# Kernel tuning notes

Measured on AMD Instinct MI355X. Metric: run time of the kernel, lower is better.

## Reference

```python
import jax, jax.numpy as jnp
import numpy as np

# ---- constants mirroring the torch module ----
LOSS_ALPHA = 1.0      # args.loss_weight_alpha (intra-class weight)
LOSS_BETA = 1.0       # args.loss_weight_beta (focal weight)
FOCAL_GAMMA = 2.0
FOCAL_ALPHA = 0.85
EPS = 1e-09
LDAM_S = 30.0
CLS_NUM = np.array([85.0, 900.0])
LDAM_MAX_M = 0.5
LDAM_W = np.array([0.15, 0.85], dtype=np.float32)
B = 16777216


def setup_inputs() -> dict:
    key = jax.random.key(0)
    k1, k2 = jax.random.split(key)
    x = jax.random.uniform(k1, (B, 2), dtype=jnp.float32)  # [B, 2] probabilities-like logits
    target = jax.random.randint(k2, (B,), 0, 2)            # binary labels
    return {"x": x, "target": target}


def _intraclass_p(centered, std, target, cls):
    # correlation between consecutive same-class rows (sorted-index order),
    # vectorized: class-c indices first via stable argsort, mask invalid pairs.
    n_rows = centered.shape[0]
    mask = target == cls
    n = jnp.sum(mask)
    order = jnp.argsort(jnp.where(mask, jnp.arange(n_rows), n_rows))
    a, b = order[:-1], order[1:]
    corr = jnp.sum(centered[a] * centered[b], axis=1) / (std[a] * std[b])
    valid = jnp.arange(n_rows - 1) < (n - 1)
    s = jnp.sum(jnp.where(valid, corr, 0.0))
    return jnp.where(n > 0, s / jnp.maximum(n, 1).astype(s.dtype), 0.0)


def reference(x, target):
    num_cls = x.shape[1]
    # ---- LDAM loss ----
    m = 1.0 / np.sqrt(np.sqrt(CLS_NUM))
    m = m * (LDAM_MAX_M / np.max(m))
    m_list = jnp.asarray(m, jnp.float32)
    w = jnp.asarray(LDAM_W)
    batch_m = m_list[target]                                      # [B]
    onehot = jax.nn.one_hot(target, num_cls, dtype=bool)          # [B, C]
    out = jnp.where(onehot, x - batch_m[:, None], x)              # margin on target logit only
    logsm = jax.nn.log_softmax(LDAM_S * out, axis=-1)
    nll = -jnp.take_along_axis(logsm, target[:, None], axis=1)[:, 0]
    wi = w[target]
    ldam = jnp.sum(wi * nll) / jnp.sum(wi)                        # weighted-mean cross entropy
    # ---- binary focal loss (treats x[:,1] as probability) ----
    p = x[:, 1]
    t = target.astype(x.dtype)
    fl = (-FOCAL_ALPHA * t * (1.0 - p) ** FOCAL_GAMMA * jnp.log(p + EPS)
          - (1.0 - FOCAL_ALPHA) * (1.0 - t) * p ** FOCAL_GAMMA * jnp.log(1.0 - p + EPS))
    focal = jnp.mean(fl)
    # ---- intra-class correlation loss ----
    centered = x - jnp.mean(x, axis=1, keepdims=True)
    std = jnp.std(x, axis=1, ddof=1)                               # torch.std default: unbiased
    p0 = _intraclass_p(centered, std, target, 0)
    p1 = _intraclass_p(centered, std, target, 1)
    intra = (p0 - p1) ** 2
    return ldam + LOSS_BETA * focal + LOSS_ALPHA * intra
```

## Files before the change

### kernel.cpp

```cpp
#include <hip/hip_runtime.h>

#define E_BLOCK 8192
#define E_WAVE  2048
#define ITERS   16

#define M1      0.2771814156f
#define LDAM_S  30.0f

struct BlockRec {
  int s0, p0, s1, p1;
  float wnll, fl;
  int cnt1, pad;
};

__device__ __forceinline__ void comb(int &sa, int &pa, int sb, int pb) {
  if (pa == 0) { sa = sb; pa = pb; }
  else if (pb != 0) {
    int la = ((pa >> 1) & 1) * 2 - 1;
    int fb = (pb & 1) * 2 - 1;
    sa += sb + la * fb;
    pa = 4 | (pa & 1) | (pb & 2);
  }
}

__global__ __launch_bounds__(256) void loss_pass1(
    const float* __restrict__ x, const int* __restrict__ tgt,
    BlockRec* __restrict__ recs, int B) {
  const int w    = threadIdx.x >> 6;
  const int lane = threadIdx.x & 63;
  const int waveBase = blockIdx.x * E_BLOCK + w * E_WAVE;

  float wnll = 0.f, fls = 0.f;
  int cnt1 = 0;
  int rs0 = 0, rp0 = 0, rs1 = 0, rp1 = 0;

  for (int j = 0; j < ITERS; ++j) {
    const int e = waveBase + ((j << 6) + lane) * 2;
    int ps0 = 0, pp0 = 0, ps1 = 0, pp1 = 0;
    if (e < B) {
      const float4 xv = *reinterpret_cast<const float4*>(x + 2 * e);
      const int2  tv = *reinterpret_cast<const int2*>(tgt + e);
      int sA, sB;
      {
        const float x0 = xv.x, x1 = xv.y; const int t = tv.x;
        const float d  = t ? LDAM_S * (x0 - x1 + M1) : LDAM_S * (x1 - x0 + 0.5f);
        const float sp = fmaxf(d, 0.f) + __logf(1.f + __expf(-fabsf(d)));
        wnll += (t ? 0.85f : 0.15f) * sp;
        fls  += t ? (-0.85f * (1.f - x1) * (1.f - x1) * __logf(x1 + 1e-9f))
                  : (-0.15f * x1 * x1 * __logf(1.f - x1 + 1e-9f));
        cnt1 += t;
        sA = (x0 > x1) ? 1 : -1;
      }
      {
        const float x0 = xv.z, x1 = xv.w; const int t = tv.y;
        const float d  = t ? LDAM_S * (x0 - x1 + M1) : LDAM_S * (x1 - x0 + 0.5f);
        const float sp = fmaxf(d, 0.f) + __logf(1.f + __expf(-fabsf(d)));
        wnll += (t ? 0.85f : 0.15f) * sp;
        fls  += t ? (-0.85f * (1.f - x1) * (1.f - x1) * __logf(x1 + 1e-9f))
                  : (-0.15f * x1 * x1 * __logf(1.f - x1 + 1e-9f));
        cnt1 += t;
        sB = (x0 > x1) ? 1 : -1;
      }
      const int bA = (sA > 0), bB = (sB > 0);
      const bool a0 = (tv.x == 0), b0 = (tv.y == 0);
      if (a0 && b0)      { ps0 = sA * sB; pp0 = 4 | bA | (bB << 1); }
      else if (a0)       { pp0 = 4 | bA | (bA << 1); }
      else if (b0)       { pp0 = 4 | bB | (bB << 1); }
      if (!a0 && !b0)    { ps1 = sA * sB; pp1 = 4 | bA | (bB << 1); }
      else if (!a0)      { pp1 = 4 | bA | (bA << 1); }
      else if (!b0)      { pp1 = 4 | bB | (bB << 1); }
    }
    #pragma unroll
    for (int k = 0; k < 6; ++k) {
      const int m = 1 << k;
      const int os0 = __shfl_xor(ps0, m), op0 = __shfl_xor(pp0, m);
      const int os1 = __shfl_xor(ps1, m), op1 = __shfl_xor(pp1, m);
      const bool up = (lane & m) != 0;
      int fs = up ? os0 : ps0, fp = up ? op0 : pp0;
      int gs = up ? ps0 : os0, gp = up ? pp0 : op0;
      comb(fs, fp, gs, gp); ps0 = fs; pp0 = fp;
      fs = up ? os1 : ps1; fp = up ? op1 : pp1;
      gs = up ? ps1 : os1; gp = up ? pp1 : op1;
      comb(fs, fp, gs, gp); ps1 = fs; pp1 = fp;
    }
    comb(rs0, rp0, ps0, pp0);
    comb(rs1, rp1, ps1, pp1);
  }

  #pragma unroll
  for (int k = 1; k < 64; k <<= 1) {
    wnll += __shfl_xor(wnll, k);
    fls  += __shfl_xor(fls, k);
    cnt1 += __shfl_xor(cnt1, k);
  }

  __shared__ int   shi[4][5];
  __shared__ float shf[4][2];
  if (lane == 0) {
    shi[w][0] = rs0; shi[w][1] = rp0; shi[w][2] = rs1; shi[w][3] = rp1; shi[w][4] = cnt1;
    shf[w][0] = wnll; shf[w][1] = fls;
  }
  __syncthreads();
  if (threadIdx.x == 0) {
    int S0 = 0, P0 = 0, S1 = 0, P1 = 0, C = 0; float W = 0.f, F = 0.f;
    #pragma unroll
    for (int q = 0; q < 4; ++q) {
      comb(S0, P0, shi[q][0], shi[q][1]);
      comb(S1, P1, shi[q][2], shi[q][3]);
      C += shi[q][4]; W += shf[q][0]; F += shf[q][1];
    }
    BlockRec r; r.s0 = S0; r.p0 = P0; r.s1 = S1; r.p1 = P1;
    r.wnll = W; r.fl = F; r.cnt1 = C; r.pad = 0;
    recs[blockIdx.x] = r;
  }
}

__global__ __launch_bounds__(64) void loss_pass2(
    const BlockRec* __restrict__ recs, int NB, int B, float* __restrict__ out) {
  const int lane = threadIdx.x;
  const int G = (NB + 63) >> 6;
  int s0 = 0, p0 = 0, s1 = 0, p1 = 0;
  double W = 0.0, F = 0.0;
  long long C = 0;
  for (int g = 0; g < G; ++g) {
    const int b = lane * G + g;
    if (b < NB) {
      const BlockRec r = recs[b];
      comb(s0, p0, r.s0, r.p0);
      comb(s1, p1, r.s1, r.p1);
      W += (double)r.wnll; F += (double)r.fl; C += r.cnt1;
    }
  }
  #pragma unroll
  for (int k = 0; k < 6; ++k) {
    const int m = 1 << k;
    const int os0 = __shfl_xor(s0, m), op0 = __shfl_xor(p0, m);
    const int os1 = __shfl_xor(s1, m), op1 = __shfl_xor(p1, m);
    const double oW = __shfl_xor(W, m), oF = __shfl_xor(F, m);
    const long long oC = __shfl_xor(C, m);
    const bool up = (lane & m) != 0;
    int fs = up ? os0 : s0, fp = up ? op0 : p0;
    int gs = up ? s0 : os0, gp = up ? p0 : op0;
    comb(fs, fp, gs, gp); s0 = fs; p0 = fp;
    fs = up ? os1 : s1; fp = up ? op1 : p1;
    gs = up ? s1 : os1; gp = up ? p1 : op1;
    comb(fs, fp, gs, gp); s1 = fs; p1 = fp;
    W += oW; F += oF; C += oC;
  }
  if (lane == 0) {
    const double n1 = (double)C, n0 = (double)B - n1;
    const double sw = 0.15 * n0 + 0.85 * n1;
    const double ldam  = W / sw;
    const double focal = F / (double)B;
    const double q0 = (n0 > 0.0) ? (double)s0 / n0 : 0.0;
    const double q1 = (n1 > 0.0) ? (double)s1 / n1 : 0.0;
    const double dq = q0 - q1;
    out[0] = (float)(ldam + focal + dq * dq);
  }
}

extern "C" void kernel_launch(void* const* d_in, const int* in_sizes, int n_in,
                              void* d_out, int out_size, void* d_ws, size_t ws_size,
                              hipStream_t stream) {
  const float* x  = (const float*)d_in[0];
  const int* tgt  = (const int*)d_in[1];
  float* out      = (float*)d_out;
  const int B  = in_sizes[1];
  const int NB = (B + E_BLOCK - 1) / E_BLOCK;
  BlockRec* recs = (BlockRec*)d_ws;
  loss_pass1<<<NB, 256, 0, stream>>>(x, tgt, recs, B);
  loss_pass2<<<1, 64, 0, stream>>>(recs, NB, B, out);
}
```

Measured before the change: 254.2 us.

## Replace per-iteration wave scans with LDS-staged sequential per-thread chain reduction

Each element's sign and class are now packed into a byte and staged in shared memory. Each thread then walks a contiguous chunk of 32 elements sequentially to build per-class (sum, first, last) chain summaries. This replaces the six-step shuffle butterfly that previously ran every iteration. The second pass widens to 256 threads with a shared-memory stage and a simpler first/last combine. The aim is to cut shuffle and branch cost in the hot loop, at the price of LDS traffic and extra barriers.

```diff
diff --git a/kernel.cpp b/kernel.cpp
--- a/kernel.cpp
+++ b/kernel.cpp
@@ -13,149 +13,178 @@
   int cnt1, pad;
 };
 
-__device__ __forceinline__ void comb(int &sa, int &pa, int sb, int pb) {
-  if (pa == 0) { sa = sb; pa = pb; }
-  else if (pb != 0) {
-    int la = ((pa >> 1) & 1) * 2 - 1;
-    int fb = (pb & 1) * 2 - 1;
-    sa += sb + la * fb;
-    pa = 4 | (pa & 1) | (pb & 2);
-  }
+__device__ __forceinline__ void comb0(int &s, int &f, int &l, int sb, int fb, int lb) {
+  s += sb + l * fb;
+  f = f ? f : fb;
+  l = fb ? lb : l;
+}
+
+__device__ __forceinline__ void bfly_step(int m, int lane, int &s, int &f, int &l) {
+  const int os = __shfl_xor(s, m), of = __shfl_xor(f, m), ol = __shfl_xor(l, m);
+  const bool up = (lane & m) != 0;
+  int as = up ? os : s, af = up ? of : f, al = up ? ol : l;
+  const int bs = up ? s : os, bf = up ? f : of, bl = up ? l : ol;
+  comb0(as, af, al, bs, bf, bl);
+  s = as; f = af; l = al;
 }
 
 __global__ __launch_bounds__(256) void loss_pass1(
     const float* __restrict__ x, const int* __restrict__ tgt,
     BlockRec* __restrict__ recs, int B) {
-  const int w    = threadIdx.x >> 6;
-  const int lane = threadIdx.x & 63;
+  __shared__ unsigned int lds[3328];
+  unsigned int* chunkw = lds;
+  unsigned int* stw = lds + 2304;
+  float* wnw = (float*)(lds + 2560);
+  float* flw = (float*)(lds + 2816);
+  int*   cnw = (int*)(lds + 3072);
+  unsigned short* cs = (unsigned short*)lds;
+
+  const int tid = threadIdx.x;
+  const int w = tid >> 6, lane = tid & 63;
   const int waveBase = blockIdx.x * E_BLOCK + w * E_WAVE;
 
-  float wnll = 0.f, fls = 0.f;
-  int cnt1 = 0;
-  int rs0 = 0, rp0 = 0, rs1 = 0, rp1 = 0;
+  float wnll = 0.f, fls = 0.f; int cnt1 = 0;
 
   for (int j = 0; j < ITERS; ++j) {
     const int e = waveBase + ((j << 6) + lane) * 2;
-    int ps0 = 0, pp0 = 0, ps1 = 0, pp1 = 0;
+    unsigned int pk = 0;
     if (e < B) {
       const float4 xv = *reinterpret_cast<const float4*>(x + 2 * e);
       const int2  tv = *reinterpret_cast<const int2*>(tgt + e);
-      int sA, sB;
+      unsigned int c[2];
+      const float x0a = xv.x, x1a = xv.y; const float x0b = xv.z, x1b = xv.w;
+      const int ta = tv.x, tb = tv.y;
       {
-        const float x0 = xv.x, x1 = xv.y; const int t = tv.x;
-        const float d  = t ? LDAM_S * (x0 - x1 + M1) : LDAM_S * (x1 - x0 + 0.5f);
-        const float sp = fmaxf(d, 0.f) + __logf(1.f + __expf(-fabsf(d)));
-        wnll += (t ? 0.85f : 0.15f) * sp;
-        fls  += t ? (-0.85f * (1.f - x1) * (1.f - x1) * __logf(x1 + 1e-9f))
-                  : (-0.15f * x1 * x1 * __logf(1.f - x1 + 1e-9f));
-        cnt1 += t;
-        sA = (x0 > x1) ? 1 : -1;
+        const float d  = x0a - x1a;
+        const float z  = LDAM_S * (ta ? (d + M1) : (0.5f - d));
+        const float sp = fmaxf(z, 0.f) + __logf(1.f + __expf(-fabsf(z)));
+        wnll += (ta ? 0.85f : 0.15f) * sp;
+        const float p  = x1a;
+        const float lg = __logf((ta ? p : (1.f - p)) + 1e-9f);
+        const float cf = ta ? (-0.85f * (1.f - p) * (1.f - p)) : (-0.15f * p * p);
+        fls += cf * lg;
+        cnt1 += ta;
+        c[0] = 4u | (unsigned)(x0a > x1a) | ((unsigned)ta << 1);
       }
       {
-        const float x0 = xv.z, x1 = xv.w; const int t = tv.y;
-        const float d  = t ? LDAM_S * (x0 - x1 + M1) : LDAM_S * (x1 - x0 + 0.5f);
-        const float sp = fmaxf(d, 0.f) + __logf(1.f + __expf(-fabsf(d)));
-        wnll += (t ? 0.85f : 0.15f) * sp;
-        fls  += t ? (-0.85f * (1.f - x1) * (1.f - x1) * __logf(x1 + 1e-9f))
-                  : (-0.15f * x1 * x1 * __logf(1.f - x1 + 1e-9f));
-        cnt1 += t;
-        sB = (x0 > x1) ? 1 : -1;
+        const float d  = x0b - x1b;
+        const float z  = LDAM_S * (tb ? (d + M1) : (0.5f - d));
+        const float sp = fmaxf(z, 0.f) + __logf(1.f + __expf(-fabsf(z)));
+        wnll += (tb ? 0.85f : 0.15f) * sp;
+        const float p  = x1b;
+        const float lg = __logf((tb ? p : (1.f - p)) + 1e-9f);
+        const float cf = tb ? (-0.85f * (1.f - p) * (1.f - p)) : (-0.15f * p * p);
+        fls += cf * lg;
+        cnt1 += tb;
+        c[1] = 4u | (unsigned)(x0b > x1b) | ((unsigned)tb << 1);
       }
-      const int bA = (sA > 0), bB = (sB > 0);
-      const bool a0 = (tv.x == 0), b0 = (tv.y == 0);
-      if (a0 && b0)      { ps0 = sA * sB; pp0 = 4 | bA | (bB << 1); }
-      else if (a0)       { pp0 = 4 | bA | (bA << 1); }
-      else if (b0)       { pp0 = 4 | bB | (bB << 1); }
-      if (!a0 && !b0)    { ps1 = sA * sB; pp1 = 4 | bA | (bB << 1); }
-      else if (!a0)      { pp1 = 4 | bA | (bA << 1); }
-      else if (!b0)      { pp1 = 4 | bB | (bB << 1); }
+      pk = c[0] | (c[1] << 8);
+    }
+    const int li2 = w * 1024 + (j << 6) + lane;
+    cs[(li2 >> 4) * 18 + (li2 & 15)] = (unsigned short)pk;
+  }
+  __syncthreads();
+
+  int s0 = 0, f0 = 0, l0 = 0, s1 = 0, f1 = 0, l1 = 0;
+  #pragma unroll
+  for (int r = 0; r < 8; ++r) {
+    const unsigned int wv = chunkw[tid * 9 + r];
+    #pragma unroll
+    for (int k = 0; k < 4; ++k) {
+      const unsigned int b = (wv >> (8 * k)) & 7u;
+      if (b & 4u) {
+        const int sv = (int)((b & 1u) << 1) - 1;
+        const int t  = (int)((b >> 1) & 1u);
+        const int lv = t ? l1 : l0;
+        const int add = lv * sv;
+        if (t) { s1 += add; l1 = sv; f1 = f1 ? f1 : sv; }
+        else   { s0 += add; l0 = sv; f0 = f0 ? f0 : sv; }
+      }
+    }
+  }
+  stw[tid] = (unsigned)(s0 + 128) | ((unsigned)(f0 + 1) << 8) | ((unsigned)(l0 + 1) << 10)
+           | ((unsigned)(s1 + 128) << 16) | ((unsigned)(f1 + 1) << 24) | ((unsigned)(l1 + 1) << 26);
+  wnw[tid] = wnll; flw[tid] = fls; cnw[tid] = cnt1;
+  __syncthreads();
+
+  if (w == 0) {
+    int S0 = 0, F0 = 0, L0 = 0, S1 = 0, F1 = 0, L1 = 0;
+    float W = 0.f, F = 0.f; int C = 0;
+    #pragma unroll
+    for (int q = 0; q < 4; ++q) {
+      const int i = lane * 4 + q;
+      const unsigned int pk = stw[i];
+      comb0(S0, F0, L0, (int)(pk & 255u) - 128, (int)((pk >> 8) & 3u) - 1, (int)((pk >> 10) & 3u) - 1);
+      comb0(S1, F1, L1, (int)((pk >> 16) & 255u) - 128, (int)((pk >> 24) & 3u) - 1, (int)((pk >> 26) & 3u) - 1);
+      W += wnw[i]; F += flw[i]; C += cnw[i];
     }
     #pragma unroll
     for (int k = 0; k < 6; ++k) {
       const int m = 1 << k;
-      const int os0 = __shfl_xor(ps0, m), op0 = __shfl_xor(pp0, m);
-      const int os1 = __shfl_xor(ps1, m), op1 = __shfl_xor(pp1, m);
-      const bool up = (lane & m) != 0;
-      int fs = up ? os0 : ps0, fp = up ? op0 : pp0;
-      int gs = up ? ps0 : os0, gp = up ? pp0 : op0;
-      comb(fs, fp, gs, gp); ps0 = fs; pp0 = fp;
-      fs = up ? os1 : ps1; fp = up ? op1 : pp1;
-      gs = up ? ps1 : os1; gp = up ? pp1 : op1;
-      comb(fs, fp, gs, gp); ps1 = fs; pp1 = fp;
-    }
-    comb(rs0, rp0, ps0, pp0);
-    comb(rs1, rp1, ps1, pp1);
-  }
-
-  #pragma unroll
-  for (int k = 1; k < 64; k <<= 1) {
-    wnll += __shfl_xor(wnll, k);
-    fls  += __shfl_xor(fls, k);
-    cnt1 += __shfl_xor(cnt1, k);
-  }
-
-  __shared__ int   shi[4][5];
-  __shared__ float shf[4][2];
-  if (lane == 0) {
-    shi[w][0] = rs0; shi[w][1] = rp0; shi[w][2] = rs1; shi[w][3] = rp1; shi[w][4] = cnt1;
-    shf[w][0] = wnll; shf[w][1] = fls;
-  }
+      bfly_step(m, lane, S0, F0, L0);
+      bfly_step(m, lane, S1, F1, L1);
+      W += __shfl_xor(W, m); F += __shfl_xor(F, m); C += __shfl_xor(C, m);
+    }
+    if (lane == 0) {
+      BlockRec r;
+      r.s0 = S0; r.p0 = (F0 + 1) | ((L0 + 1) << 4);
+      r.s1 = S1; r.p1 = (F1 + 1) | ((L1 + 1) << 4);
+      r.wnll = W; r.fl = F; r.cnt1 = C; r.pad = 0;
+      recs[blockIdx.x] = r;
+    }
+  }
+}
+
+__global__ __launch_bounds__(256) void loss_pass2(
+    const BlockRec* __restrict__ recs, int NB, int B, float* __restrict__ out) {
+  __shared__ int sS0[256], sF0[256], sL0[256], sS1[256], sF1[256], sL1[256], sC[256];
+  __shared__ double sW[256], sFl[256];
+  const int tid = threadIdx.x, w = tid >> 6, lane = tid & 63;
+  const int R = (NB + 255) >> 8;
+
+  int s0 = 0, f0 = 0, l0 = 0, s1 = 0, f1 = 0, l1 = 0;
+  double W = 0.0, Fd = 0.0; int C = 0;
+  for (int r = 0; r < R; ++r) {
+    const int b = tid * R + r;
+    if (b < NB) {
+      const BlockRec rec = recs[b];
+      comb0(s0, f0, l0, rec.s0, (rec.p0 & 3) - 1, ((rec.p0 >> 4) & 3) - 1);
+      comb0(s1, f1, l1, rec.s1, (rec.p1 & 3) - 1, ((rec.p1 >> 4) & 3) - 1);
+      W += (double)rec.wnll; Fd += (double)rec.fl; C += rec.cnt1;
+    }
+  }
+  sS0[tid] = s0; sF0[tid] = f0; sL0[tid] = l0;
+  sS1[tid] = s1; sF1[tid] = f1; sL1[tid] = l1;
+  sC[tid] = C; sW[tid] = W; sFl[tid] = Fd;
   __syncthreads();
-  if (threadIdx.x == 0) {
-    int S0 = 0, P0 = 0, S1 = 0, P1 = 0, C = 0; float W = 0.f, F = 0.f;
+
+  if (w == 0) {
+    int S0 = 0, F0 = 0, L0 = 0, S1 = 0, F1 = 0, L1 = 0; int Ct = 0;
+    double Wt = 0.0, Ft = 0.0;
     #pragma unroll
     for (int q = 0; q < 4; ++q) {
-      comb(S0, P0, shi[q][0], shi[q][1]);
-      comb(S1, P1, shi[q][2], shi[q][3]);
-      C += shi[q][4]; W += shf[q][0]; F += shf[q][1];
-    }
-    BlockRec r; r.s0 = S0; r.p0 = P0; r.s1 = S1; r.p1 = P1;
-    r.wnll = W; r.fl = F; r.cnt1 = C; r.pad = 0;
-    recs[blockIdx.x] = r;
-  }
-}
-
-__global__ __launch_bounds__(64) void loss_pass2(
-    const BlockRec* __restrict__ recs, int NB, int B, float* __restrict__ out) {
-  const int lane = threadIdx.x;
-  const int G = (NB + 63) >> 6;
-  int s0 = 0, p0 = 0, s1 = 0, p1 = 0;
-  double W = 0.0, F = 0.0;
-  long long C = 0;
-  for (int g = 0; g < G; ++g) {
-    const int b = lane * G + g;
-    if (b < NB) {
-      const BlockRec r = recs[b];
-      comb(s0, p0, r.s0, r.p0);
-      comb(s1, p1, r.s1, r.p1);
-      W += (double)r.wnll; F += (double)r.fl; C += r.cnt1;
-    }
-  }
-  #pragma unroll
-  for (int k = 0; k < 6; ++k) {
-    const int m = 1 << k;
-    const int os0 = __shfl_xor(s0, m), op0 = __shfl_xor(p0, m);
-    const int os1 = __shfl_xor(s1, m), op1 = __shfl_xor(p1, m);
-    const double oW = __shfl_xor(W, m), oF = __shfl_xor(F, m);
-    const long long oC = __shfl_xor(C, m);
-    const bool up = (lane & m) != 0;
-    int fs = up ? os0 : s0, fp = up ? op0 : p0;
-    int gs = up ? s0 : os0, gp = up ? p0 : op0;
-    comb(fs, fp, gs, gp); s0 = fs; p0 = fp;
-    fs = up ? os1 : s1; fp = up ? op1 : p1;
-    gs = up ? s1 : os1; gp = up ? p1 : op1;
-    comb(fs, fp, gs, gp); s1 = fs; p1 = fp;
-    W += oW; F += oF; C += oC;
-  }
-  if (lane == 0) {
-    const double n1 = (double)C, n0 = (double)B - n1;
-    const double sw = 0.15 * n0 + 0.85 * n1;
-    const double ldam  = W / sw;
-    const double focal = F / (double)B;
-    const double q0 = (n0 > 0.0) ? (double)s0 / n0 : 0.0;
-    const double q1 = (n1 > 0.0) ? (double)s1 / n1 : 0.0;
-    const double dq = q0 - q1;
-    out[0] = (float)(ldam + focal + dq * dq);
+      const int i = lane * 4 + q;
+      comb0(S0, F0, L0, sS0[i], sF0[i], sL0[i]);
+      comb0(S1, F1, L1, sS1[i], sF1[i], sL1[i]);
+      Wt += sW[i]; Ft += sFl[i]; Ct += sC[i];
+    }
+    #pragma unroll
+    for (int k = 0; k < 6; ++k) {
+      const int m = 1 << k;
+      bfly_step(m, lane, S0, F0, L0);
+      bfly_step(m, lane, S1, F1, L1);
+      Wt += __shfl_xor(Wt, m); Ft += __shfl_xor(Ft, m); Ct += __shfl_xor(Ct, m);
+    }
+    if (lane == 0) {
+      const double n1 = (double)Ct, n0 = (double)B - n1;
+      const double sw = 0.15 * n0 + 0.85 * n1;
+      const double ldam  = Wt / sw;
+      const double focal = Ft / (double)B;
+      const double q0 = (n0 > 0.0) ? (double)S0 / n0 : 0.0;
+      const double q1 = (n1 > 0.0) ? (double)S1 / n1 : 0.0;
+      const double dq = q0 - q1;
+      out[0] = (float)(ldam + focal + dq * dq);
+    }
   }
 }
 
@@ -169,5 +198,5 @@
   const int NB = (B + E_BLOCK - 1) / E_BLOCK;
   BlockRec* recs = (BlockRec*)d_ws;
   loss_pass1<<<NB, 256, 0, stream>>>(x, tgt, recs, B);
-  loss_pass2<<<1, 64, 0, stream>>>(recs, NB, B, out);
-}
+  loss_pass2<<<1, 256, 0, stream>>>(recs, NB, B, out);
+}
```

After: 245.0 us. 3.6% less time.
